# Performance work log

Measured on AMD Instinct MI355X. Metric: run time of the kernel, lower is better.

Reference implementation:

```python
import jax, jax.numpy as jnp
import numpy as np
from jax import lax

HIDDEN = 1024; HEADS = 16; HEAD = 64; LAYERS = 4; MLP = 4096
PATCH = 16; TUBE = 2; CROP = 224; FRAMES = 16
GRID = CROP // PATCH          # 14
DEPTH = FRAMES // TUBE        # 8
N_TOK = DEPTH * GRID * GRID   # 1568
EPS = 1e-6
D_ROT = 2 * ((HEAD // 3) // 2)  # 20 per rotary axis (d, h, w); 4 dims left unrotated


def setup_inputs() -> dict:
    key = jax.random.key(0)
    ks = jax.random.split(key, 12)
    w = lambda k, shape: jax.random.normal(k, shape, jnp.float32) * 0.02
    L, H, M = LAYERS, HIDDEN, MLP
    return {
        "pixel_values_videos": jax.random.normal(ks[0], (2, FRAMES, 3, CROP, CROP), jnp.float32),
        "patch_w": w(ks[1], (H, 3, TUBE, PATCH, PATCH)),  # Conv3d OIDHW
        "patch_b": jnp.zeros((H,), jnp.float32),
        "ln1_g": jnp.ones((L, H), jnp.float32), "ln1_b": jnp.zeros((L, H), jnp.float32),
        "qw": w(ks[2], (L, H, H)), "qb": jnp.zeros((L, H), jnp.float32),
        "kw": w(ks[3], (L, H, H)), "kb": jnp.zeros((L, H), jnp.float32),
        "vw": w(ks[4], (L, H, H)), "vb": jnp.zeros((L, H), jnp.float32),
        "pw": w(ks[5], (L, H, H)), "pb": jnp.zeros((L, H), jnp.float32),
        "ln2_g": jnp.ones((L, H), jnp.float32), "ln2_b": jnp.zeros((L, H), jnp.float32),
        "fc1w": w(ks[6], (L, M, H)), "fc1b": jnp.zeros((L, M), jnp.float32),
        "fc2w": w(ks[7], (L, H, M)), "fc2b": jnp.zeros((L, H), jnp.float32),
        "lnf_g": jnp.ones((H,), jnp.float32), "lnf_b": jnp.zeros((H,), jnp.float32),
    }


def _layer_norm(x, g, b):
    mu = jnp.mean(x, axis=-1, keepdims=True)
    var = jnp.mean(jnp.square(x - mu), axis=-1, keepdims=True)
    return (x - mu) * lax.rsqrt(var + EPS) * g + b


def _position_ids():
    ids = jnp.arange(N_TOK)
    tpf = GRID * GRID
    d_pos = ids // tpf
    rem = ids - d_pos * tpf
    h_pos = rem // GRID
    w_pos = rem - h_pos * GRID
    return d_pos, h_pos, w_pos


def _rotate(x, pos):
    # x: (B, H, N, D); matches VJEPA2 rotate_queries_or_keys:
    # tiled (not interleaved) sin/cos * interleaved rotate-half.
    D = x.shape[-1]
    omega = 1.0 / (10000.0 ** (jnp.arange(D // 2, dtype=x.dtype) / (D / 2.0)))
    freq = pos.astype(x.dtype)[:, None] * omega              # (N, D/2)
    sin = jnp.concatenate([jnp.sin(freq)] * 2, axis=-1)      # (N, D) tiled (torch .repeat)
    cos = jnp.concatenate([jnp.cos(freq)] * 2, axis=-1)
    y = x.reshape(x.shape[:-1] + (D // 2, 2))
    y = jnp.stack([-y[..., 1], y[..., 0]], axis=-1).reshape(x.shape)
    return x * cos + y * sin


def _apply_rope(x, pos_ids):
    d_pos, h_pos, w_pos = pos_ids
    s0, s1, s2 = 0, D_ROT, 2 * D_ROT
    parts = [_rotate(x[..., s0:s1], d_pos), _rotate(x[..., s1:s2], h_pos),
             _rotate(x[..., s2:3 * D_ROT], w_pos)]
    if 3 * D_ROT < HEAD:
        parts.append(x[..., 3 * D_ROT:])
    return jnp.concatenate(parts, axis=-1)


def _forward(pixel_values_videos, patch_w, patch_b, ln1_g, ln1_b, qw, qb, kw, kb,
             vw, vb, pw, pb, ln2_g, ln2_b, fc1w, fc1b, fc2w, fc2b, lnf_g, lnf_b):
    B = pixel_values_videos.shape[0]
    x = jnp.transpose(pixel_values_videos, (0, 2, 1, 3, 4))  # (B, C, T, H, W)
    h = lax.conv_general_dilated(x, patch_w, window_strides=(TUBE, PATCH, PATCH),
                                 padding="VALID",
                                 dimension_numbers=("NCDHW", "OIDHW", "NCDHW"))
    h = h + patch_b[None, :, None, None, None]
    h = h.reshape(B, HIDDEN, -1).transpose(0, 2, 1)          # (B, N, HIDDEN)

    pos_ids = _position_ids()
    scale = HEAD ** -0.5

    for i in range(LAYERS):
        # attention block
        xn = _layer_norm(h, ln1_g[i], ln1_b[i])
        def heads(w_, b_):
            return (xn @ w_.T + b_).reshape(B, N_TOK, HEADS, HEAD).transpose(0, 2, 1, 3)
        q = _apply_rope(heads(qw[i], qb[i]), pos_ids)
        k = _apply_rope(heads(kw[i], kb[i]), pos_ids)
        v = heads(vw[i], vb[i])
        aw = jnp.einsum("bhnd,bhmd->bhnm", q, k) * scale
        aw = jax.nn.softmax(aw.astype(jnp.float32), axis=-1).astype(q.dtype)
        o = jnp.einsum("bhnm,bhmd->bhnd", aw, v)
        o = o.transpose(0, 2, 1, 3).reshape(B, N_TOK, HIDDEN)
        h = h + (o @ pw[i].T + pb[i])
        # MLP block
        xn = _layer_norm(h, ln2_g[i], ln2_b[i])
        m = jax.nn.gelu(xn @ fc1w[i].T + fc1b[i], approximate=False)
        h = h + (m @ fc2w[i].T + fc2b[i])

    return _layer_norm(h, lnf_g, lnf_b)


def reference(pixel_values_videos, patch_w, patch_b, ln1_g, ln1_b, qw, qb, kw, kb,
              vw, vb, pw, pb, ln2_g, ln2_b, fc1w, fc1b, fc2w, fc2b, lnf_g, lnf_b):
    return _forward(pixel_values_videos, patch_w, patch_b, ln1_g, ln1_b, qw, qb, kw, kb,
                    vw, vb, pw, pb, ln2_g, ln2_b, fc1w, fc1b, fc2w, fc2b, lnf_g, lnf_b)
```

## Files before the change

### kernel.cpp

```cpp
#include <hip/hip_runtime.h>
#include <math.h>

#define NTOK   1568
#define BATCH  2
#define HID    1024
#define MLPD   4096
#define NLAYER 4
#define ROWS   (BATCH*NTOK)
#define CONVK  1536

typedef __bf16 bf16x8 __attribute__((ext_vector_type(8)));
typedef float  f32x4  __attribute__((ext_vector_type(4)));

__device__ __forceinline__ unsigned short f2b(float f) {
  unsigned int u = __float_as_uint(f);
  unsigned int r = u + 0x7FFFu + ((u >> 16) & 1u);
  return (unsigned short)(r >> 16);
}
__device__ __forceinline__ float b2f(unsigned short s) {
  return __uint_as_float((unsigned int)s << 16);
}

__device__ __forceinline__ void async16(const unsigned short* g, unsigned short* l) {
  __builtin_amdgcn_global_load_lds(
      (__attribute__((address_space(1))) void*)(void*)g,
      (__attribute__((address_space(3))) void*)(void*)l, 16, 0, 0);
}

__global__ __launch_bounds__(256) void cast4_k(const float* __restrict__ s,
                                               unsigned short* __restrict__ d,
                                               long long n4) {
  long long i = (long long)blockIdx.x * 256 + threadIdx.x;
  long long stride = (long long)gridDim.x * 256;
  for (; i < n4; i += stride) {
    float4 v = ((const float4*)s)[i];
    *(ushort4*)(d + i * 4) = make_ushort4(f2b(v.x), f2b(v.y), f2b(v.z), f2b(v.w));
  }
}

__global__ __launch_bounds__(256) void castqkv_k(const float* __restrict__ q,
                                                 const float* __restrict__ k,
                                                 const float* __restrict__ v,
                                                 unsigned short* __restrict__ dst) {
  const float* src = blockIdx.y == 0 ? q : (blockIdx.y == 1 ? k : v);
  long long i4 = (long long)blockIdx.x * 256 + threadIdx.x;
  long long e = i4 * 4;
  int layer = (int)(e >> 20);
  long long de = e + ((long long)(2 * layer + blockIdx.y) << 20);
  float4 val = ((const float4*)src)[i4];
  *(ushort4*)(dst + de) = make_ushort4(f2b(val.x), f2b(val.y), f2b(val.z), f2b(val.w));
}

__global__ __launch_bounds__(256) void biascat_k(const float* __restrict__ qb,
                                                 const float* __restrict__ kb,
                                                 const float* __restrict__ vb,
                                                 float* __restrict__ dst) {
  int idx = blockIdx.x * 256 + threadIdx.x;
  int layer = idx / 3072, c = idx % 3072;
  float v = c < 1024 ? qb[layer * 1024 + c]
            : (c < 2048 ? kb[layer * 1024 + c - 1024] : vb[layer * 1024 + c - 2048]);
  dst[idx] = v;
}

__global__ __launch_bounds__(256) void im2col_k(const float* __restrict__ pv,
                                                unsigned short* __restrict__ A) {
  int idx = blockIdx.x * 256 + threadIdx.x;
  int row = idx / CONVK, col = idx % CONVK;
  int b = row / NTOK, t = row % NTOK;
  int d = t / 196, r = t % 196, hh = r / 14, ww = r % 14;
  int c = col >> 9, r2 = col & 511, td = r2 >> 8, ph = (r2 >> 4) & 15, pw = r2 & 15;
  int frame = 2 * d + td;
  const float* src = pv + ((((long long)b * 16 + frame) * 3 + c) * 224 + (hh * 16 + ph)) * 224
                        + (ww * 16 + pw);
  A[idx] = f2b(*src);
}

__global__ __launch_bounds__(256) void gemm_bt(const unsigned short* __restrict__ A,
                                               const unsigned short* __restrict__ B,
                                               unsigned short* outP,
                                               int M, int N, int K, int kChunk,
                                               size_t zStride) {
  __shared__ unsigned short As[2][128 * 32];
  __shared__ unsigned short Bs[2][128 * 32];
  const int tid = threadIdx.x;
  const int lane = tid & 63;
  const int w = tid >> 6;
  const int wm = (w >> 1) * 64, wn = (w & 1) * 64;
  const int l15 = lane & 15, l4 = lane >> 4;
  const int bm = blockIdx.y, bn = blockIdx.x;
  const int wbase = tid & ~63;
  const int kbeg = blockIdx.z * kChunk;

  auto stage = [&](int buf, int k0) {
#pragma unroll
    for (int it = 0; it < 2; ++it) {
      int c = it * 256 + tid;
      int rowA = bm * 128 + (c >> 2);
      if (rowA >= M) rowA = M - 1;
      async16(A + (size_t)rowA * K + k0 + (c & 3) * 8, &As[buf][(it * 256 + wbase) * 8]);
      int rowB = bn * 128 + (c >> 2);
      async16(B + (size_t)rowB * K + k0 + (c & 3) * 8, &Bs[buf][(it * 256 + wbase) * 8]);
    }
  };

  f32x4 acc[4][4] = {};
  stage(0, kbeg);
  const int nIter = kChunk >> 5;

  for (int i = 0; i < nIter; ++i) {
    const int cur = i & 1;
    __syncthreads();
    if (i + 1 < nIter) stage(cur ^ 1, kbeg + (i + 1) * 32);

    bf16x8 af[4], bfr[4];
#pragma unroll
    for (int ii = 0; ii < 4; ++ii)
      af[ii] = *(const bf16x8*)&As[cur][(wm + ii * 16 + l15) * 32 + l4 * 8];
#pragma unroll
    for (int j = 0; j < 4; ++j)
      bfr[j] = *(const bf16x8*)&Bs[cur][(wn + j * 16 + l15) * 32 + l4 * 8];
#pragma unroll
    for (int ii = 0; ii < 4; ++ii)
#pragma unroll
      for (int j = 0; j < 4; ++j)
        acc[ii][j] = __builtin_amdgcn_mfma_f32_16x16x32_bf16(af[ii], bfr[j], acc[ii][j], 0, 0, 0);
  }

  unsigned short* pout = outP + (size_t)blockIdx.z * zStride;
#pragma unroll
  for (int ii = 0; ii < 4; ++ii) {
    int rowb = bm * 128 + wm + ii * 16 + l4 * 4;
#pragma unroll
    for (int r = 0; r < 4; ++r) {
      int rr = rowb + r;
      if (rr >= M) continue;
#pragma unroll
      for (int j = 0; j < 4; ++j) {
        int col = bn * 128 + wn + j * 16 + l15;
        pout[(size_t)rr * N + col] = f2b(acc[ii][j][r]);
      }
    }
  }
}

template <int NP, int GELU>
__global__ __launch_bounds__(256) void reduceN_k(const unsigned short* p,
                                                 const float* __restrict__ bias,
                                                 unsigned short* outB,
                                                 int MN, int N, size_t pStride) {
  int i8 = blockIdx.x * 256 + threadIdx.x;
  int e = i8 * 8;
  float acc[8];
#pragma unroll
  for (int j = 0; j < 8; ++j) acc[j] = 0.0f;
#pragma unroll
  for (int pp = 0; pp < NP; ++pp) {
    const unsigned short* src = p + (size_t)pp * pStride + e;
    ushort4 a0 = *(const ushort4*)src;
    ushort4 a1 = *(const ushort4*)(src + 4);
    acc[0] += b2f(a0.x); acc[1] += b2f(a0.y); acc[2] += b2f(a0.z); acc[3] += b2f(a0.w);
    acc[4] += b2f(a1.x); acc[5] += b2f(a1.y); acc[6] += b2f(a1.z); acc[7] += b2f(a1.w);
  }
  int col = e % N;
  float4 b0 = *(const float4*)(bias + col);
  float4 b1 = *(const float4*)(bias + col + 4);
  acc[0] += b0.x; acc[1] += b0.y; acc[2] += b0.z; acc[3] += b0.w;
  acc[4] += b1.x; acc[5] += b1.y; acc[6] += b1.z; acc[7] += b1.w;
  if (GELU) {
#pragma unroll
    for (int j = 0; j < 8; ++j)
      acc[j] = 0.5f * acc[j] * (1.0f + erff(acc[j] * 0.70710678118654752f));
  }
  *(ushort4*)(outB + e) = make_ushort4(f2b(acc[0]), f2b(acc[1]), f2b(acc[2]), f2b(acc[3]));
  *(ushort4*)(outB + e + 4) = make_ushort4(f2b(acc[4]), f2b(acc[5]), f2b(acc[6]), f2b(acc[7]));
}

template <int NP, int RESID, int FINAL>
__global__ __launch_bounds__(256) void redln_k(const unsigned short* __restrict__ p,
                                               const float* __restrict__ bias,
                                               const float* resid,
                                               const float* __restrict__ g,
                                               const float* __restrict__ b,
                                               float* hOut,
                                               unsigned short* __restrict__ xnOut,
                                               float* __restrict__ fOut,
                                               size_t pStride) {
  __shared__ float red[8];
  const int row = blockIdx.x, tid = threadIdx.x;
  const int col = tid * 4;
  const size_t off = (size_t)row * HID + col;
  float v0 = 0, v1 = 0, v2 = 0, v3 = 0;
#pragma unroll
  for (int pp = 0; pp < NP; ++pp) {
    ushort4 a = *(const ushort4*)(p + (size_t)pp * pStride + off);
    v0 += b2f(a.x); v1 += b2f(a.y); v2 += b2f(a.z); v3 += b2f(a.w);
  }
  float4 bs = *(const float4*)(bias + col);
  v0 += bs.x; v1 += bs.y; v2 += bs.z; v3 += bs.w;
  if (RESID) {
    float4 r = *(const float4*)(resid + off);
    v0 += r.x; v1 += r.y; v2 += r.z; v3 += r.w;
  }
  if (!FINAL) *(float4*)(hOut + off) = make_float4(v0, v1, v2, v3);
  float s = v0 + v1 + v2 + v3;
  float q = v0 * v0 + v1 * v1 + v2 * v2 + v3 * v3;
  for (int o2 = 32; o2; o2 >>= 1) { s += __shfl_xor(s, o2); q += __shfl_xor(q, o2); }
  if ((tid & 63) == 0) { red[tid >> 6] = s; red[4 + (tid >> 6)] = q; }
  __syncthreads();
  float ts = red[0] + red[1] + red[2] + red[3];
  float tq = red[4] + red[5] + red[6] + red[7];
  float mu = ts * (1.0f / HID);
  float var = tq * (1.0f / HID) - mu * mu;
  float rs = rsqrtf(var + 1e-6f);
  float o0 = (v0 - mu) * rs * g[col + 0] + b[col + 0];
  float o1 = (v1 - mu) * rs * g[col + 1] + b[col + 1];
  float o2 = (v2 - mu) * rs * g[col + 2] + b[col + 2];
  float o3 = (v3 - mu) * rs * g[col + 3] + b[col + 3];
  if (FINAL) {
    *(float4*)(fOut + off) = make_float4(o0, o1, o2, o3);
  } else {
    *(ushort4*)(xnOut + off) = make_ushort4(f2b(o0), f2b(o1), f2b(o2), f2b(o3));
  }
}

__global__ __launch_bounds__(256) void qkvprep_k(const unsigned short* __restrict__ qkvb,
                                                 unsigned short* __restrict__ Qh,
                                                 unsigned short* __restrict__ Kh,
                                                 unsigned short* __restrict__ VT) {
  __shared__ unsigned short Vs[64 * 72];
  const int tile = blockIdx.x, bh = blockIdx.y;
  const int b = bh >> 4, head = bh & 15;
  const int tid = threadIdx.x;
  const int tl = tid >> 2, dc = tid & 3;
  const int tg = tile * 64 + tl;
  const int trc = tg < NTOK ? tg : NTOK - 1;
  const bool valid = tg < NTOK;
  const size_t srow = ((size_t)(b * NTOK + trc)) * 3072 + head * 64 + dc * 16;

  {
    uint4 v0 = *(const uint4*)(qkvb + srow + 2048);
    uint4 v1 = *(const uint4*)(qkvb + srow + 2048 + 8);
    *(uint4*)&Vs[tl * 72 + dc * 16] = v0;
    *(uint4*)&Vs[tl * 72 + dc * 16 + 8] = v1;
  }

  const int t = trc;
  const int dpos = t / 196, rem = t - dpos * 196, hpos = rem / 14, wpos = rem - hpos * 14;
  const float LG = 0.9210340371976184f;
  union V16 { uint4 u[2]; unsigned short s[16]; };
  V16 qin, kin, qout, kout;
  qin.u[0] = *(const uint4*)(qkvb + srow);
  qin.u[1] = *(const uint4*)(qkvb + srow + 8);
  kin.u[0] = *(const uint4*)(qkvb + srow + 1024);
  kin.u[1] = *(const uint4*)(qkvb + srow + 1024 + 8);
#pragma unroll
  for (int p = 0; p < 8; ++p) {
    int d0 = dc * 16 + 2 * p;
    float qx0 = b2f(qin.s[2 * p]), qx1 = b2f(qin.s[2 * p + 1]);
    float kx0 = b2f(kin.s[2 * p]), kx1 = b2f(kin.s[2 * p + 1]);
    float qo0, qo1, ko0, ko1;
    if (d0 >= 60) { qo0 = qx0; qo1 = qx1; ko0 = kx0; ko1 = kx1; }
    else {
      int region = d0 / 20;
      int j0 = d0 - region * 20;
      int pos = region == 0 ? dpos : (region == 1 ? hpos : wpos);
      float fp = (float)pos;
      int i0 = j0 % 10, i1 = (j0 + 1) % 10;
      float f0 = expf(-LG * (float)i0) * fp;
      float f1 = expf(-LG * (float)i1) * fp;
      float c0 = cosf(f0), s0 = sinf(f0), c1 = cosf(f1), s1 = sinf(f1);
      qo0 = qx0 * c0 - qx1 * s0; qo1 = qx1 * c1 + qx0 * s1;
      ko0 = kx0 * c0 - kx1 * s0; ko1 = kx1 * c1 + kx0 * s1;
    }
    qout.s[2 * p]     = f2b(qo0 * 0.125f);
    qout.s[2 * p + 1] = f2b(qo1 * 0.125f);
    kout.s[2 * p]     = f2b(ko0);
    kout.s[2 * p + 1] = f2b(ko1);
  }
  if (valid) {
    size_t drow = ((size_t)bh * NTOK + tg) * 64 + dc * 16;
    *(uint4*)(Qh + drow)     = qout.u[0];
    *(uint4*)(Qh + drow + 8) = qout.u[1];
    *(uint4*)(Kh + drow)     = kout.u[0];
    *(uint4*)(Kh + drow + 8) = kout.u[1];
  }
  __syncthreads();
  {
    int d = tid >> 2, tc = tid & 3;
    if (tile * 64 + tc * 16 < NTOK) {
      V16 o;
#pragma unroll
      for (int jj = 0; jj < 16; ++jj) o.s[jj] = Vs[(tc * 16 + jj) * 72 + d];
      unsigned short* dst = VT + ((size_t)bh * 64 + d) * NTOK + tile * 64 + tc * 16;
      *(uint4*)dst = o.u[0];
      *(uint4*)(dst + 8) = o.u[1];
    }
  }
}

__global__ __launch_bounds__(256, 4) void flash5_k(const unsigned short* __restrict__ Qh,
                                                   const unsigned short* __restrict__ Kh,
                                                   const unsigned short* __restrict__ VT,
                                                   unsigned short* __restrict__ Opart,
                                                   float2* __restrict__ ml) {
  __shared__ unsigned short Ks[2][64 * 64];
  __shared__ unsigned short Vs[2][64 * 64];
  const int bh = blockIdx.x, qt = blockIdx.y, kv = blockIdx.z;
  const int kt0 = kv ? 13 : 0, kt1 = kv ? 25 : 13;
  const int tid = threadIdx.x, lane = tid & 63, w = tid >> 6;
  const int l15 = lane & 15, l4 = lane >> 4;
  const size_t hb = (size_t)bh * NTOK * 64;
  const unsigned short* kgp = Kh + hb;
  const unsigned short* vbp = VT + (size_t)bh * 64 * NTOK;

  const int srow0 = w * 8 + (lane >> 3);
  const int scg0  = (lane & 7) ^ (srow0 & 7);
  const int srow1 = srow0 + 32;
  const int scg1  = (lane & 7) ^ (srow1 & 7);

  const int qrow = qt * 64 + w * 16 + l15;
  const int qrc = qrow < NTOK ? qrow : NTOK - 1;
  bf16x8 q0 = *(const bf16x8*)(Qh + hb + (size_t)qrc * 64 + l4 * 8);
  bf16x8 q1 = *(const bf16x8*)(Qh + hb + (size_t)qrc * 64 + 32 + l4 * 8);

  f32x4 oacc[4] = {};
  float m = -1e30f, l = 0.0f;

  {
    const int kc0 = kt0 * 64;
    async16(kgp + (size_t)(kc0 + srow0) * 64 + scg0 * 8, &Ks[0][(size_t)w * 512]);
    async16(kgp + (size_t)(kc0 + srow1) * 64 + scg1 * 8, &Ks[0][(size_t)(w + 4) * 512]);
    async16(vbp + (size_t)srow0 * NTOK + kc0 + scg0 * 8, &Vs[0][(size_t)w * 512]);
    async16(vbp + (size_t)srow1 * NTOK + kc0 + scg1 * 8, &Vs[0][(size_t)(w + 4) * 512]);
  }

  const int h7 = l15 & 7;
  const int p1 = (l4 ^ h7) * 8;
  const int p2 = ((l4 + 4) ^ h7) * 8;

  for (int kt = kt0; kt < kt1; ++kt) {
    const int cur = (kt - kt0) & 1, nxt = cur ^ 1;
    const int kb = kt * 64;
    __syncthreads();

    if (kt + 1 < kt1) {
      const int kn = kb + 64;
      async16(kgp + (size_t)(kn + srow0) * 64 + scg0 * 8, &Ks[nxt][(size_t)w * 512]);
      async16(kgp + (size_t)(kn + srow1) * 64 + scg1 * 8, &Ks[nxt][(size_t)(w + 4) * 512]);
      async16(vbp + (size_t)srow0 * NTOK + kn + scg0 * 8, &Vs[nxt][(size_t)w * 512]);
      async16(vbp + (size_t)srow1 * NTOK + kn + scg1 * 8, &Vs[nxt][(size_t)(w + 4) * 512]);
    }

    bf16x8 kc0[4], kc1[4];
#pragma unroll
    for (int nt = 0; nt < 4; ++nt) {
      const unsigned short* kr = &Ks[cur][(nt * 16 + l15) * 64];
      kc0[nt] = *(const bf16x8*)(kr + p1);
      kc1[nt] = *(const bf16x8*)(kr + p2);
    }
    f32x4 s[4] = {};
#pragma unroll
    for (int nt = 0; nt < 4; ++nt) {
      s[nt] = __builtin_amdgcn_mfma_f32_16x16x32_bf16(kc0[nt], q0, s[nt], 0, 0, 0);
      s[nt] = __builtin_amdgcn_mfma_f32_16x16x32_bf16(kc1[nt], q1, s[nt], 0, 0, 0);
    }
    bf16x8 vf0[4], vf1[4];
#pragma unroll
    for (int dt = 0; dt < 4; ++dt) {
      const unsigned short* vr = &Vs[cur][(dt * 16 + l15) * 64];
      vf0[dt] = *(const bf16x8*)(vr + p1);
      vf1[dt] = *(const bf16x8*)(vr + p2);
    }

    if (kb + 64 > NTOK) {
#pragma unroll
      for (int nt = 0; nt < 4; ++nt)
#pragma unroll
        for (int r = 0; r < 4; ++r)
          if (kb + nt * 16 + l4 * 4 + r >= NTOK) s[nt][r] = -1e30f;
    }
    float rmax = s[0][0];
#pragma unroll
    for (int nt = 0; nt < 4; ++nt)
#pragma unroll
      for (int r = 0; r < 4; ++r) rmax = fmaxf(rmax, s[nt][r]);
    rmax = fmaxf(rmax, __shfl_xor(rmax, 16));
    rmax = fmaxf(rmax, __shfl_xor(rmax, 32));
    float mn = fmaxf(m, rmax);
    float alpha = __expf(m - mn);
    m = mn;
    float rsum = 0.0f;
#pragma unroll
    for (int nt = 0; nt < 4; ++nt)
#pragma unroll
      for (int r = 0; r < 4; ++r) {
        float p = __expf(s[nt][r] - mn);
        s[nt][r] = p;
        rsum += p;
      }
    rsum += __shfl_xor(rsum, 16);
    rsum += __shfl_xor(rsum, 32);
    l = l * alpha + rsum;
#pragma unroll
    for (int dt = 0; dt < 4; ++dt)
#pragma unroll
      for (int r = 0; r < 4; ++r) oacc[dt][r] *= alpha;

    unsigned pk01[4], pk23[4];
#pragma unroll
    for (int nt = 0; nt < 4; ++nt) {
      pk01[nt] = (unsigned)f2b(s[nt][0]) | ((unsigned)f2b(s[nt][1]) << 16);
      pk23[nt] = (unsigned)f2b(s[nt][2]) | ((unsigned)f2b(s[nt][3]) << 16);
    }
    const int srcA = ((l4 & 1) << 5) | l15;
    const int srcB = srcA + 16;
    const bool hi = (l4 >> 1) != 0;
    union PB { unsigned u[4]; bf16x8 v; } pf[2];
#pragma unroll
    for (int kc = 0; kc < 2; ++kc) {
      unsigned t0, t1;
      t0 = __shfl(pk01[2 * kc], srcA); t1 = __shfl(pk01[2 * kc + 1], srcA);
      pf[kc].u[0] = hi ? t1 : t0;
      t0 = __shfl(pk23[2 * kc], srcA); t1 = __shfl(pk23[2 * kc + 1], srcA);
      pf[kc].u[1] = hi ? t1 : t0;
      t0 = __shfl(pk01[2 * kc], srcB); t1 = __shfl(pk01[2 * kc + 1], srcB);
      pf[kc].u[2] = hi ? t1 : t0;
      t0 = __shfl(pk23[2 * kc], srcB); t1 = __shfl(pk23[2 * kc + 1], srcB);
      pf[kc].u[3] = hi ? t1 : t0;
    }
#pragma unroll
    for (int dt = 0; dt < 4; ++dt) {
      oacc[dt] = __builtin_amdgcn_mfma_f32_16x16x32_bf16(vf0[dt], pf[0].v, oacc[dt], 0, 0, 0);
      oacc[dt] = __builtin_amdgcn_mfma_f32_16x16x32_bf16(vf1[dt], pf[1].v, oacc[dt], 0, 0, 0);
    }
  }

  __syncthreads();
  unsigned short* Os = &Ks[0][0];
#pragma unroll
  for (int dt = 0; dt < 4; ++dt)
#pragma unroll
    for (int r = 0; r < 4; ++r)
      Os[w * 1152 + l15 * 72 + dt * 16 + l4 * 4 + r] = f2b(oacc[dt][r]);
  if (qrow < NTOK) {
    uint4 a  = *(const uint4*)&Os[w * 1152 + l15 * 72 + l4 * 16];
    uint4 bq = *(const uint4*)&Os[w * 1152 + l15 * 72 + l4 * 16 + 8];
    unsigned short* op = Opart + ((size_t)(kv * 32 + bh) * NTOK + qrow) * 64;
    *(uint4*)(op + l4 * 16) = a;
    *(uint4*)(op + l4 * 16 + 8) = bq;
    if (l4 == 0) ml[(size_t)(kv * 32 + bh) * NTOK + qrow] = make_float2(m, l);
  }
}

__global__ __launch_bounds__(256) void fcomb_k(const unsigned short* __restrict__ Op,
                                               const float2* __restrict__ ml,
                                               unsigned short* __restrict__ O) {
  const int bh = blockIdx.x, qt = blockIdx.y;
  const int tid = threadIdx.x;
  const int qr = qt * 64 + (tid >> 2);
  const int dc = (tid & 3) * 16;
  if (qr >= NTOK) return;
  const int b = bh >> 4, head = bh & 15;
  float2 a0 = ml[(size_t)bh * NTOK + qr];
  float2 a1 = ml[(size_t)(32 + bh) * NTOK + qr];
  float M = fmaxf(a0.x, a1.x);
  float w0 = __expf(a0.x - M), w1 = __expf(a1.x - M);
  float inv = 1.0f / (a0.y * w0 + a1.y * w1);
  w0 *= inv; w1 *= inv;
  union V16 { uint4 u[2]; unsigned short s[16]; } p0, p1, o;
  const unsigned short* q0 = Op + ((size_t)bh * NTOK + qr) * 64 + dc;
  const unsigned short* q1 = Op + ((size_t)(32 + bh) * NTOK + qr) * 64 + dc;
  p0.u[0] = *(const uint4*)q0;       p0.u[1] = *(const uint4*)(q0 + 8);
  p1.u[0] = *(const uint4*)q1;       p1.u[1] = *(const uint4*)(q1 + 8);
#pragma unroll
  for (int j = 0; j < 16; ++j) o.s[j] = f2b(b2f(p0.s[j]) * w0 + b2f(p1.s[j]) * w1);
  unsigned short* dst = O + ((size_t)(b * NTOK + qr)) * HID + head * 64 + dc;
  *(uint4*)dst = o.u[0];
  *(uint4*)(dst + 8) = o.u[1];
}

extern "C" void kernel_launch(void* const* d_in, const int* in_sizes, int n_in,
                              void* d_out, int out_size, void* d_ws, size_t ws_size,
                              hipStream_t stream) {
  (void)in_sizes; (void)n_in; (void)out_size; (void)ws_size;
  const float* pv      = (const float*)d_in[0];
  const float* patch_w = (const float*)d_in[1];
  const float* patch_b = (const float*)d_in[2];
  const float* ln1_g   = (const float*)d_in[3];
  const float* ln1_b   = (const float*)d_in[4];
  const float* qw = (const float*)d_in[5];
  const float* qb = (const float*)d_in[6];
  const float* kw = (const float*)d_in[7];
  const float* kb = (const float*)d_in[8];
  const float* vw = (const float*)d_in[9];
  const float* vb = (const float*)d_in[10];
  const float* pw = (const float*)d_in[11];
  const float* pb = (const float*)d_in[12];
  const float* ln2_g = (const float*)d_in[13];
  const float* ln2_b = (const float*)d_in[14];
  const float* fc1w = (const float*)d_in[15];
  const float* fc1b = (const float*)d_in[16];
  const float* fc2w = (const float*)d_in[17];
  const float* fc2b = (const float*)d_in[18];
  const float* lnf_g = (const float*)d_in[19];
  const float* lnf_b = (const float*)d_in[20];

  char* wsp = (char*)d_ws;
  auto alloc = [&](size_t bytes) {
    char* p = wsp;
    wsp += (bytes + 255) & ~(size_t)255;
    return p;
  };
  unsigned short* wPatch = (unsigned short*)alloc((size_t)1024 * 1536 * 2);
  unsigned short* wQKV   = (unsigned short*)alloc((size_t)NLAYER * 3072 * 1024 * 2);
  unsigned short* wP     = (unsigned short*)alloc((size_t)NLAYER * HID * HID * 2);
  unsigned short* wF1    = (unsigned short*)alloc((size_t)NLAYER * MLPD * HID * 2);
  unsigned short* wF2    = (unsigned short*)alloc((size_t)NLAYER * HID * MLPD * 2);
  float*          qkvbias = (float*)alloc((size_t)NLAYER * 3072 * 4);
  unsigned short* Aim  = (unsigned short*)alloc((size_t)ROWS * CONVK * 2);
  float*          h    = (float*)alloc((size_t)ROWS * HID * 4);
  unsigned short* xnb  = (unsigned short*)alloc((size_t)ROWS * HID * 2);
  unsigned short* qkvo = (unsigned short*)alloc((size_t)ROWS * 3072 * 2);
  unsigned short* Qh   = (unsigned short*)alloc((size_t)ROWS * HID * 2 + 8192);
  unsigned short* Kh   = (unsigned short*)alloc((size_t)ROWS * HID * 2 + 8192);
  unsigned short* VT   = (unsigned short*)alloc((size_t)ROWS * HID * 2 + 8192);
  unsigned short* ob   = (unsigned short*)alloc((size_t)ROWS * HID * 2);
  unsigned short* mb   = (unsigned short*)alloc((size_t)ROWS * MLPD * 2);

  unsigned short* part  = Qh;
  unsigned short* partM = mb;
  unsigned short* Opart = mb;
  float2*         mlbuf = (float2*)(mb + (size_t)2 * 32 * NTOK * 64);
  const size_t MNs = (size_t)ROWS * HID;
  const size_t strideF1 = (size_t)(mb - part);

  auto cast = [&](const float* s, unsigned short* d, long long n) {
    long long n4 = n / 4;
    int grid = (int)((n4 + 255) / 256);
    if (grid > 16384) grid = 16384;
    cast4_k<<<grid, 256, 0, stream>>>(s, d, n4);
  };
  cast(patch_w, wPatch, (long long)1024 * 1536);
  castqkv_k<<<dim3(4096, 3), 256, 0, stream>>>(qw, kw, vw, wQKV);
  cast(pw, wP, (long long)NLAYER * HID * HID);
  cast(fc1w, wF1, (long long)NLAYER * MLPD * HID);
  cast(fc2w, wF2, (long long)NLAYER * HID * MLPD);
  biascat_k<<<48, 256, 0, stream>>>(qb, kb, vb, qkvbias);

  im2col_k<<<(ROWS * CONVK) / 256, 256, 0, stream>>>(pv, Aim);
  gemm_bt<<<dim3(8, 25, 3), 256, 0, stream>>>(Aim, wPatch, part, ROWS, HID, CONVK, 512, MNs);
  redln_k<3, 0, 0><<<ROWS, 256, 0, stream>>>(
      part, patch_b, nullptr, ln1_g, ln1_b, h, xnb, nullptr, MNs);

  for (int i = 0; i < NLAYER; ++i) {
    gemm_bt<<<dim3(24, 25, 2), 256, 0, stream>>>(
        xnb, wQKV + (size_t)i * 3072 * 1024, part, ROWS, 3072, HID, 512,
        (size_t)ROWS * 3072);
    reduceN_k<2, 0><<<(ROWS * 3072) / 2048, 256, 0, stream>>>(
        part, qkvbias + i * 3072, qkvo, ROWS * 3072, 3072, (size_t)ROWS * 3072);
    qkvprep_k<<<dim3(25, 32), 256, 0, stream>>>(qkvo, Qh, Kh, VT);
    flash5_k<<<dim3(32, 25, 2), 256, 0, stream>>>(Qh, Kh, VT, Opart, mlbuf);
    fcomb_k<<<dim3(32, 25), 256, 0, stream>>>(Opart, mlbuf, ob);
    gemm_bt<<<dim3(8, 25, 4), 256, 0, stream>>>(
        ob, wP + (size_t)i * HID * HID, partM, ROWS, HID, HID, 256, MNs);
    redln_k<4, 1, 0><<<ROWS, 256, 0, stream>>>(
        partM, pb + i * HID, h, ln2_g + i * HID, ln2_b + i * HID, h, xnb, nullptr, MNs);
    gemm_bt<<<dim3(32, 25, 2), 256, 0, stream>>>(
        xnb, wF1 + (size_t)i * MLPD * HID, part, ROWS, MLPD, HID, 512, strideF1);
    reduceN_k<2, 1><<<(ROWS * MLPD) / 2048, 256, 0, stream>>>(
        part, fc1b + i * MLPD, mb, ROWS * MLPD, MLPD, strideF1);
    gemm_bt<<<dim3(8, 25, 4), 256, 0, stream>>>(
        mb, wF2 + (size_t)i * HID * MLPD, part, ROWS, HID, MLPD, 1024, MNs);
    if (i < NLAYER - 1) {
      redln_k<4, 1, 0><<<ROWS, 256, 0, stream>>>(
          part, fc2b + i * HID, h, ln1_g + (i + 1) * HID, ln1_b + (i + 1) * HID,
          h, xnb, nullptr, MNs);
    } else {
      redln_k<4, 1, 1><<<ROWS, 256, 0, stream>>>(
          part, fc2b + i * HID, h, lnf_g, lnf_b, nullptr, nullptr, (float*)d_out, MNs);
    }
  }
}
```

Before: 1.404 ms.

## Use exp2 softmax with folded log2e scale, lazy rescale, and MFMA priority

Folds log2(e) into the query scale so the flash-attention softmax and the split combine can use the hardware exp2 directly. Rescaling of the running max, sum and output accumulator is skipped when no lane's new row max exceeds the old one by more than a threshold, which saves a multiply pass over the accumulators. It also adds s_setprio around the MFMA blocks and uses the native packed bf16 conversion for the probabilities. The lazy rescale lets probabilities grow up to 2^11.5 before renormalising, so bf16 precision is relied on over a wider range of values.

Result: no change. 1.390 ms (-0.9%).

```diff
diff --git a/kernel.cpp b/kernel.cpp
--- a/kernel.cpp
+++ b/kernel.cpp
@@ -10,6 +10,7 @@
 #define CONVK  1536
 
 typedef __bf16 bf16x8 __attribute__((ext_vector_type(8)));
+typedef __bf16 bf16x2 __attribute__((ext_vector_type(2)));
 typedef float  f32x4  __attribute__((ext_vector_type(4)));
 
 __device__ __forceinline__ unsigned short f2b(float f) {
@@ -20,6 +21,13 @@
 __device__ __forceinline__ float b2f(unsigned short s) {
   return __uint_as_float((unsigned int)s << 16);
 }
+__device__ __forceinline__ unsigned cvt2(float a, float b) {
+  bf16x2 t;
+  t[0] = (__bf16)a;
+  t[1] = (__bf16)b;
+  return __builtin_bit_cast(unsigned, t);
+}
+__device__ __forceinline__ float e2(float x) { return __builtin_amdgcn_exp2f(x); }
 
 __device__ __forceinline__ void async16(const unsigned short* g, unsigned short* l) {
   __builtin_amdgcn_global_load_lds(
@@ -272,8 +280,9 @@
       qo0 = qx0 * c0 - qx1 * s0; qo1 = qx1 * c1 + qx0 * s1;
       ko0 = kx0 * c0 - kx1 * s0; ko1 = kx1 * c1 + kx0 * s1;
     }
-    qout.s[2 * p]     = f2b(qo0 * 0.125f);
-    qout.s[2 * p + 1] = f2b(qo1 * 0.125f);
+    const float QS = 0.18033688011112042f;
+    qout.s[2 * p]     = f2b(qo0 * QS);
+    qout.s[2 * p + 1] = f2b(qo1 * QS);
     kout.s[2 * p]     = f2b(ko0);
     kout.s[2 * p + 1] = f2b(ko1);
   }
@@ -359,11 +368,13 @@
       kc1[nt] = *(const bf16x8*)(kr + p2);
     }
     f32x4 s[4] = {};
+    __builtin_amdgcn_s_setprio(1);
 #pragma unroll
     for (int nt = 0; nt < 4; ++nt) {
       s[nt] = __builtin_amdgcn_mfma_f32_16x16x32_bf16(kc0[nt], q0, s[nt], 0, 0, 0);
       s[nt] = __builtin_amdgcn_mfma_f32_16x16x32_bf16(kc1[nt], q1, s[nt], 0, 0, 0);
     }
+    __builtin_amdgcn_s_setprio(0);
     bf16x8 vf0[4], vf1[4];
 #pragma unroll
     for (int dt = 0; dt < 4; ++dt) {
@@ -386,31 +397,34 @@
       for (int r = 0; r < 4; ++r) rmax = fmaxf(rmax, s[nt][r]);
     rmax = fmaxf(rmax, __shfl_xor(rmax, 16));
     rmax = fmaxf(rmax, __shfl_xor(rmax, 32));
-    float mn = fmaxf(m, rmax);
-    float alpha = __expf(m - mn);
-    m = mn;
+    if (!__all(rmax - m <= 11.5f)) {
+      float mn = fmaxf(m, rmax);
+      float alpha = e2(m - mn);
+      m = mn;
+      l *= alpha;
+#pragma unroll
+      for (int dt = 0; dt < 4; ++dt)
+#pragma unroll
+        for (int r = 0; r < 4; ++r) oacc[dt][r] *= alpha;
+    }
     float rsum = 0.0f;
 #pragma unroll
     for (int nt = 0; nt < 4; ++nt)
 #pragma unroll
       for (int r = 0; r < 4; ++r) {
-        float p = __expf(s[nt][r] - mn);
+        float p = e2(s[nt][r] - m);
         s[nt][r] = p;
         rsum += p;
       }
     rsum += __shfl_xor(rsum, 16);
     rsum += __shfl_xor(rsum, 32);
-    l = l * alpha + rsum;
-#pragma unroll
-    for (int dt = 0; dt < 4; ++dt)
-#pragma unroll
-      for (int r = 0; r < 4; ++r) oacc[dt][r] *= alpha;
+    l += rsum;
 
     unsigned pk01[4], pk23[4];
 #pragma unroll
     for (int nt = 0; nt < 4; ++nt) {
-      pk01[nt] = (unsigned)f2b(s[nt][0]) | ((unsigned)f2b(s[nt][1]) << 16);
-      pk23[nt] = (unsigned)f2b(s[nt][2]) | ((unsigned)f2b(s[nt][3]) << 16);
+      pk01[nt] = cvt2(s[nt][0], s[nt][1]);
+      pk23[nt] = cvt2(s[nt][2], s[nt][3]);
     }
     const int srcA = ((l4 & 1) << 5) | l15;
     const int srcB = srcA + 16;
@@ -428,11 +442,13 @@
       t0 = __shfl(pk23[2 * kc], srcB); t1 = __shfl(pk23[2 * kc + 1], srcB);
       pf[kc].u[3] = hi ? t1 : t0;
     }
+    __builtin_amdgcn_s_setprio(1);
 #pragma unroll
     for (int dt = 0; dt < 4; ++dt) {
       oacc[dt] = __builtin_amdgcn_mfma_f32_16x16x32_bf16(vf0[dt], pf[0].v, oacc[dt], 0, 0, 0);
       oacc[dt] = __builtin_amdgcn_mfma_f32_16x16x32_bf16(vf1[dt], pf[1].v, oacc[dt], 0, 0, 0);
     }
+    __builtin_amdgcn_s_setprio(0);
   }
 
   __syncthreads();
@@ -464,7 +480,7 @@
   float2 a0 = ml[(size_t)bh * NTOK + qr];
   float2 a1 = ml[(size_t)(32 + bh) * NTOK + qr];
   float M = fmaxf(a0.x, a1.x);
-  float w0 = __expf(a0.x - M), w1 = __expf(a1.x - M);
+  float w0 = e2(a0.x - M), w1 = e2(a1.x - M);
   float inv = 1.0f / (a0.y * w0 + a1.y * w1);
   w0 *= inv; w1 *= inv;
   union V16 { uint4 u[2]; unsigned short s[16]; } p0, p1, o;
```
